# Kernel optimization log

Measured on AMD Instinct MI355X. Metric: run time of the kernel, lower is better.

## Reference

```python
import jax, jax.numpy as jnp
import numpy as np

N = 10000   # nodes
E = 160000  # edges (avg degree 16)
IN = 512
HID = 512
OUT = 512


def setup_inputs() -> dict:
    key = jax.random.key(0)
    ks = jax.random.split(key, 8)
    x = jax.random.normal(ks[0], (N, IN), dtype=jnp.float32)
    edge_index = jax.random.randint(ks[1], (2, E), 0, N, dtype=jnp.int64)
    def w(k, fi, fo):
        return jax.random.normal(k, (fi, fo), dtype=jnp.float32) * (1.0 / np.sqrt(fi)).astype(np.float32)
    return {
        "x": x,
        "edge_index": edge_index,
        "W1": w(ks[2], IN, HID), "b1": jnp.zeros((HID,), jnp.float32),
        "W2": w(ks[3], HID, HID), "b2": jnp.zeros((HID,), jnp.float32),
        "W3": w(ks[4], HID, OUT), "b3": jnp.zeros((OUT,), jnp.float32),
    }


def _gcn_norm(edge_index, n):
    # add self loops, then symmetric normalization D^{-1/2} (A+I) D^{-1/2}
    loops = jnp.arange(n, dtype=edge_index.dtype)
    row = jnp.concatenate([edge_index[0], loops])  # source
    col = jnp.concatenate([edge_index[1], loops])  # target (aggregation dim)
    deg = jax.ops.segment_sum(jnp.ones_like(col, jnp.float32), col, num_segments=n)
    dis = jnp.where(deg > 0, jax.lax.rsqrt(jnp.maximum(deg, 1.0)), 0.0)
    norm = dis[row] * dis[col]  # [E+N]
    return row, col, norm


def _gcn_layer(x, row, col, norm, W, b, n):
    h = x @ W                                    # [N, d_out] dense GEMM
    msg = h[row] * norm[:, None]                 # gather + scale, [E+N, d_out]
    out = jax.ops.segment_sum(msg, col, num_segments=n)  # scatter-add
    return out + b


def reference(x, edge_index, W1, b1, W2, b2, W3, b3):
    n = x.shape[0]
    row, col, norm = _gcn_norm(edge_index, n)
    h = _gcn_layer(x, row, col, norm, W1, b1, n)
    h = jax.nn.relu(h)  # dropout is identity in eval mode
    h = _gcn_layer(h, row, col, norm, W2, b2, n)
    h = jax.nn.relu(h)
    h = _gcn_layer(h, row, col, norm, W3, b3, n)
    return h
```

## Files before the change

kernel.cpp:

```cpp
#include <hip/hip_runtime.h>

typedef __attribute__((ext_vector_type(8))) short bf16x8;
typedef __attribute__((ext_vector_type(4))) float f32x4;

#define N_NODES 10000
#define N_EDGES 160000
#define FDIM    512
#define ELL     64
#define BM 64
#define BN 128
#define BK 64
#define TM 157
#define NGEMM (TM * 4)
#define NSCAT 625
#define NTRAN 768

__device__ __forceinline__ float bf2f(unsigned int u) {
    union { unsigned int i; float f; } v; v.i = u << 16; return v.f;
}
__device__ __forceinline__ float bfs2f(short s) {
    return bf2f((unsigned int)(unsigned short)s);
}
__device__ __forceinline__ unsigned short f2bf(float f) {
    union { float f; unsigned int u; } v; v.f = f;
    unsigned int u = v.u;
    unsigned int r = u + 0x7fffu + ((u >> 16) & 1u);
    return (unsigned short)(r >> 16);
}
__device__ __forceinline__ void gload_lds16(const void* g, void* l) {
    __builtin_amdgcn_global_load_lds(
        (const __attribute__((address_space(1))) unsigned int*)g,
        (__attribute__((address_space(3))) unsigned int*)l, 16, 0, 0);
}
__device__ __forceinline__ int wave_is_f32(const unsigned int* w) {
    unsigned int v = w[(size_t)(threadIdx.x & 63) * 1000];
    unsigned int ex = (v >> 7) & 0xFFu;
    unsigned long long inb = __ballot(ex >= 100u && ex <= 140u);
    return (__popcll(inb) >= 48) ? 0 : 1;
}

__global__ __launch_bounds__(256) void prep_v6(
        const void* __restrict__ x, const void* __restrict__ ei,
        const void* __restrict__ W1, const void* __restrict__ W2,
        const void* __restrict__ W3, unsigned short* __restrict__ Wt,
        int* __restrict__ cnt, int* __restrict__ flags) {
    int b = blockIdx.x;
    if (b < NTRAN) {
        __shared__ unsigned short tile[32][33];
        int z = b >> 8, t = b & 255;
        const void* W = (z == 0) ? W1 : (z == 1) ? W2 : W3;
        unsigned short* out = Wt + (size_t)z * FDIM * FDIM;
        int ff32 = wave_is_f32((const unsigned int*)W);
        int tx = threadIdx.x & 31, ty = threadIdx.x >> 5;
        int xcol = (t & 15) * 32 + tx;
        int y0 = (t >> 4) * 32 + ty;
        #pragma unroll
        for (int j = 0; j < 32; j += 8) {
            int idx = (y0 + j) * FDIM + xcol;
            unsigned short v = ff32 ? f2bf(((const float*)W)[idx])
                                    : ((const unsigned short*)W)[idx];
            tile[ty + j][tx] = v;
        }
        __syncthreads();
        int x2 = (t >> 4) * 32 + tx;
        int y2 = (t & 15) * 32 + ty;
        #pragma unroll
        for (int j = 0; j < 32; j += 8)
            out[(y2 + j) * FDIM + x2] = tile[tx][ty + j];
    } else if (b < NTRAN + NSCAT) {
        const unsigned long long* e64 = (const unsigned long long*)ei;
        unsigned long long v = e64[(size_t)(threadIdx.x & 63) * 2500];
        unsigned long long big = __ballot(v > 0xFFFFFFFFull);
        int i64 = (big == 0ull);
        int e = (b - NTRAN) * 256 + threadIdx.x;
        int c = i64 ? (int)((const long long*)ei)[N_EDGES + e]
                    : ((const int*)ei)[N_EDGES + e];
        atomicAdd(&cnt[c], 1);
    } else {
        if (threadIdx.x < 64) {
            const unsigned long long* e64 = (const unsigned long long*)ei;
            unsigned long long v = e64[(size_t)threadIdx.x * 2500];
            unsigned long long big = __ballot(v > 0xFFFFFFFFull);
            const unsigned int* xw = (const unsigned int*)x;
            unsigned int w = xw[(size_t)threadIdx.x * 1000];
            unsigned int ex = (w >> 7) & 0xFFu;
            unsigned long long inb = __ballot(ex >= 100u && ex <= 140u);
            if (threadIdx.x == 0) {
                flags[0] = (big == 0ull) ? 1 : 0;
                flags[1] = (__popcll(inb) >= 48) ? 0 : 1;
            }
        }
    }
}

__global__ __launch_bounds__(256) void gemm_scat_v6(
        const void* __restrict__ Ap, const unsigned short* __restrict__ Bt,
        unsigned short* __restrict__ C, int M, int a_ext,
        const int* __restrict__ flags, const void* __restrict__ ei,
        const int* __restrict__ cnt, int* __restrict__ cursor,
        int2* __restrict__ ell, int do_scatter) {
    __shared__ unsigned short As[BM * BK];
    __shared__ unsigned short Bs[BN * BK];
    if (do_scatter && blockIdx.x >= NGEMM) {
        int e = (blockIdx.x - NGEMM) * 256 + threadIdx.x;
        if (e < N_EDGES) {
            int r, c;
            if (flags[0]) {
                r = (int)((const long long*)ei)[e];
                c = (int)((const long long*)ei)[N_EDGES + e];
            } else {
                r = ((const int*)ei)[e];
                c = ((const int*)ei)[N_EDGES + e];
            }
            int slot = atomicAdd(&cursor[c], 1);
            if (slot < ELL) {
                float nrm = rsqrtf((float)((cnt[r] + 1) * (cnt[c] + 1)));
                int2 pr; pr.x = r; pr.y = __float_as_int(nrm);
                ell[(size_t)c * ELL + slot] = pr;
            }
        }
        return;
    }
    const int K = FDIM;
    const int af32 = a_ext ? flags[1] : 0;
    const int tid = threadIdx.x;
    const int t = blockIdx.x;
    const int bm = (t % TM) * BM, bn = (t / TM) * BN;
    const int lane = tid & 63, wv = tid >> 6;
    const int wm = (wv >> 1) * 32, wn = (wv & 1) * 64;
    const int lrow = lane & 15, lk = (lane >> 4) * 8;
    const unsigned short* Abf = (const unsigned short*)Ap;
    f32x4 acc[2][4] = {};

    for (int k0 = 0; k0 < K; k0 += BK) {
        if (!af32) {
            #pragma unroll
            for (int j = 0; j < 2; ++j) {
                int r0 = wv * 16 + j * 8;
                int arow = bm + r0 + (lane >> 3);
                if (arow >= M) arow = M - 1;
                gload_lds16(Abf + (size_t)arow * K + k0 + (lane & 7) * 8,
                            &As[r0 * BK]);
            }
            #pragma unroll
            for (int j = 0; j < 4; ++j) {
                int r0 = wv * 32 + j * 8;
                gload_lds16(Bt + (size_t)(bn + r0 + (lane >> 3)) * K + k0 + (lane & 7) * 8,
                            &Bs[r0 * BK]);
            }
        } else {
            #pragma unroll
            for (int j = 0; j < 4; ++j) {
                int r0 = wv * 32 + j * 8;
                gload_lds16(Bt + (size_t)(bn + r0 + (lane >> 3)) * K + k0 + (lane & 7) * 8,
                            &Bs[r0 * BK]);
            }
            #pragma unroll
            for (int i = 0; i < 2; ++i) {
                int c = tid + i * 256;
                int row = c >> 3, seg = (c & 7) * 8;
                int grow = bm + row;
                bf16x8 va = {};
                if (grow < M) {
                    const float* Af = (const float*)Ap + (size_t)grow * K + k0 + seg;
                    f32x4 lo = *(const f32x4*)Af;
                    f32x4 hi = *(const f32x4*)(Af + 4);
                    #pragma unroll
                    for (int jj = 0; jj < 4; ++jj) {
                        va[jj]     = (short)f2bf(lo[jj]);
                        va[4 + jj] = (short)f2bf(hi[jj]);
                    }
                }
                *(bf16x8*)(&As[row * BK + seg]) = va;
            }
        }
        __syncthreads();
        #pragma unroll
        for (int half = 0; half < 2; ++half) {
            bf16x8 af[2], bfr[4];
            #pragma unroll
            for (int f = 0; f < 2; ++f)
                af[f] = *(const bf16x8*)(&As[(wm + f * 16 + lrow) * BK + half * 32 + lk]);
            #pragma unroll
            for (int f = 0; f < 4; ++f)
                bfr[f] = *(const bf16x8*)(&Bs[(wn + f * 16 + lrow) * BK + half * 32 + lk]);
            #pragma unroll
            for (int fm = 0; fm < 2; ++fm)
                #pragma unroll
                for (int fn = 0; fn < 4; ++fn)
                    acc[fm][fn] = __builtin_amdgcn_mfma_f32_16x16x32_bf16(
                        af[fm], bfr[fn], acc[fm][fn], 0, 0, 0);
        }
        __syncthreads();
    }

    int crow = (lane >> 4) * 4;
    int ccol = lane & 15;
    #pragma unroll
    for (int fm = 0; fm < 2; ++fm) {
        #pragma unroll
        for (int fn = 0; fn < 4; ++fn) {
            #pragma unroll
            for (int r = 0; r < 4; ++r) {
                int row = bm + wm + fm * 16 + crow + r;
                if (row < M)
                    C[(size_t)row * FDIM + bn + wn + fn * 16 + ccol] =
                        f2bf(acc[fm][fn][r]);
            }
        }
    }
}

__global__ __launch_bounds__(256) void agg_v6(
        const unsigned short* __restrict__ g, const void* __restrict__ bias,
        const int* __restrict__ cnt, const int2* __restrict__ ell,
        void* __restrict__ out, int relu, int out_ext,
        const int* __restrict__ flags) {
    int wv = threadIdx.x >> 6, lane = threadIdx.x & 63;
    int i = blockIdx.x * 2 + (wv >> 1);
    int f = (wv & 1) * 256 + lane * 4;
    float a0 = 0.f, a1 = 0.f, a2 = 0.f, a3 = 0.f;
    int ci = cnt[i];
    int rows = (ci > ELL) ? ELL : ci;
    const int2* ep = ell + (size_t)i * ELL;
    int j = 0;
    for (; j + 4 <= rows; j += 4) {
        int2 p0 = ep[j], p1 = ep[j + 1], p2 = ep[j + 2], p3 = ep[j + 3];
        uint2 v0 = *(const uint2*)(g + (size_t)p0.x * FDIM + f);
        uint2 v1 = *(const uint2*)(g + (size_t)p1.x * FDIM + f);
        uint2 v2 = *(const uint2*)(g + (size_t)p2.x * FDIM + f);
        uint2 v3 = *(const uint2*)(g + (size_t)p3.x * FDIM + f);
        float w0 = __int_as_float(p0.y), w1 = __int_as_float(p1.y);
        float w2 = __int_as_float(p2.y), w3 = __int_as_float(p3.y);
        a0 += w0 * bf2f(v0.x & 0xffffu); a1 += w0 * bf2f(v0.x >> 16);
        a2 += w0 * bf2f(v0.y & 0xffffu); a3 += w0 * bf2f(v0.y >> 16);
        a0 += w1 * bf2f(v1.x & 0xffffu); a1 += w1 * bf2f(v1.x >> 16);
        a2 += w1 * bf2f(v1.y & 0xffffu); a3 += w1 * bf2f(v1.y >> 16);
        a0 += w2 * bf2f(v2.x & 0xffffu); a1 += w2 * bf2f(v2.x >> 16);
        a2 += w2 * bf2f(v2.y & 0xffffu); a3 += w2 * bf2f(v2.y >> 16);
        a0 += w3 * bf2f(v3.x & 0xffffu); a1 += w3 * bf2f(v3.x >> 16);
        a2 += w3 * bf2f(v3.y & 0xffffu); a3 += w3 * bf2f(v3.y >> 16);
    }
    for (; j < rows; ++j) {
        int2 pp = ep[j];
        float w = __int_as_float(pp.y);
        uint2 v = *(const uint2*)(g + (size_t)pp.x * FDIM + f);
        a0 += w * bf2f(v.x & 0xffffu); a1 += w * bf2f(v.x >> 16);
        a2 += w * bf2f(v.y & 0xffffu); a3 += w * bf2f(v.y >> 16);
    }
    float wself = 1.0f / (float)(ci + 1);
    uint2 vs = *(const uint2*)(g + (size_t)i * FDIM + f);
    a0 += wself * bf2f(vs.x & 0xffffu); a1 += wself * bf2f(vs.x >> 16);
    a2 += wself * bf2f(vs.y & 0xffffu); a3 += wself * bf2f(vs.y >> 16);
    int ff32 = flags[1];
    if (ff32) {
        f32x4 bb = *(const f32x4*)((const float*)bias + f);
        a0 += bb[0]; a1 += bb[1]; a2 += bb[2]; a3 += bb[3];
    } else {
        uint2 bb = *(const uint2*)((const unsigned short*)bias + f);
        a0 += bf2f(bb.x & 0xffffu); a1 += bf2f(bb.x >> 16);
        a2 += bf2f(bb.y & 0xffffu); a3 += bf2f(bb.y >> 16);
    }
    if (relu) {
        a0 = fmaxf(a0, 0.f); a1 = fmaxf(a1, 0.f);
        a2 = fmaxf(a2, 0.f); a3 = fmaxf(a3, 0.f);
    }
    if (out_ext && ff32) {
        f32x4 o = {a0, a1, a2, a3};
        *(f32x4*)((float*)out + (size_t)i * FDIM + f) = o;
    } else {
        uint2 o;
        o.x = (unsigned int)f2bf(a0) | ((unsigned int)f2bf(a1) << 16);
        o.y = (unsigned int)f2bf(a2) | ((unsigned int)f2bf(a3) << 16);
        *(uint2*)((unsigned short*)out + (size_t)i * FDIM + f) = o;
    }
}

extern "C" void kernel_launch(void* const* d_in, const int* in_sizes, int n_in,
                              void* d_out, int out_size, void* d_ws, size_t ws_size,
                              hipStream_t stream) {
    (void)in_sizes; (void)n_in; (void)out_size; (void)ws_size;
    const void* x  = d_in[0];
    const void* ei = d_in[1];
    const void* W1 = d_in[2];
    const void* b1 = d_in[3];
    const void* W2 = d_in[4];
    const void* b2 = d_in[5];
    const void* W3 = d_in[6];
    const void* b3 = d_in[7];

    char* p = (char*)d_ws;
    auto alloc = [&](size_t bytes) -> void* {
        void* r = (void*)p;
        p += (bytes + 255) & ~(size_t)255;
        return r;
    };
    int*  flags   = (int*) alloc(16);
    int*  cntcur  = (int*) alloc((size_t)2 * N_NODES * 4);
    int2* ell     = (int2*)alloc((size_t)N_NODES * ELL * 8);
    unsigned short* Wt = (unsigned short*)alloc((size_t)3 * FDIM * FDIM * 2);
    unsigned short* g  = (unsigned short*)alloc((size_t)N_NODES * FDIM * 2);
    int* cnt    = cntcur;
    int* cursor = cntcur + N_NODES;
    unsigned short* Wt1 = Wt;
    unsigned short* Wt2 = Wt + (size_t)FDIM * FDIM;
    unsigned short* Wt3 = Wt + (size_t)2 * FDIM * FDIM;
    unsigned short* h   = (unsigned short*)d_out;

    hipMemsetAsync(cntcur, 0, (size_t)2 * N_NODES * 4, stream);
    prep_v6<<<NTRAN + NSCAT + 1, 256, 0, stream>>>(x, ei, W1, W2, W3, Wt, cnt, flags);

    gemm_scat_v6<<<NGEMM + NSCAT, 256, 0, stream>>>(x, Wt1, g, N_NODES, 1, flags,
                                                    ei, cnt, cursor, ell, 1);
    agg_v6<<<N_NODES / 2, 256, 0, stream>>>(g, b1, cnt, ell, h, 1, 0, flags);
    gemm_scat_v6<<<NGEMM, 256, 0, stream>>>(h, Wt2, g, N_NODES, 0, flags,
                                            ei, cnt, cursor, ell, 0);
    agg_v6<<<N_NODES / 2, 256, 0, stream>>>(g, b2, cnt, ell, h, 1, 0, flags);
    gemm_scat_v6<<<NGEMM, 256, 0, stream>>>(h, Wt3, g, N_NODES, 0, flags,
                                            ei, cnt, cursor, ell, 0);
    agg_v6<<<N_NODES / 2, 256, 0, stream>>>(g, b3, cnt, ell, d_out, 0, 1, flags);
}
```

Before: 226.4 us.

## Fuse aggregation with next-layer GEMM, drop count pass, swizzle LDS

Aggregation for layers 1 and 2 now runs in the same kernel as the following GEMM. Each block aggregates 48 rows into LDS and multiplies them by the full weight matrix, so the intermediate activations are never written to and reread from global memory. The separate degree-count pass and memset are gone: the scatter counts with a single atomic cursor, and edge weights are computed on the fly from counts using shuffles, which also halves the ELL storage. The GEMM's LDS layout gets an XOR swizzle to avoid bank conflicts. In exchange, the fused kernel launches only 209 blocks with a large LDS footprint, and it reloads B tiles for every block.

```diff
diff --git a/kernel.cpp b/kernel.cpp
--- a/kernel.cpp
+++ b/kernel.cpp
@@ -14,6 +14,10 @@
 #define NGEMM (TM * 4)
 #define NSCAT 625
 #define NTRAN 768
+#define NZERO 40
+#define FBM 48
+#define FNB 209
+#define APAD 520
 
 __device__ __forceinline__ float bf2f(unsigned int u) {
     union { unsigned int i; float f; } v; v.i = u << 16; return v.f;
@@ -39,53 +43,46 @@
     return (__popcll(inb) >= 48) ? 0 : 1;
 }
 
-__global__ __launch_bounds__(256) void prep_v6(
+__global__ __launch_bounds__(256) void prep_v8(
         const void* __restrict__ x, const void* __restrict__ ei,
         const void* __restrict__ W1, const void* __restrict__ W2,
         const void* __restrict__ W3, unsigned short* __restrict__ Wt,
         int* __restrict__ cnt, int* __restrict__ flags) {
-    int b = blockIdx.x;
+    int b = blockIdx.x, tid = threadIdx.x;
     if (b < NTRAN) {
         __shared__ unsigned short tile[32][33];
         int z = b >> 8, t = b & 255;
         const void* W = (z == 0) ? W1 : (z == 1) ? W2 : W3;
-        unsigned short* out = Wt + (size_t)z * FDIM * FDIM;
+        unsigned short* outp = Wt + (size_t)z * FDIM * FDIM;
         int ff32 = wave_is_f32((const unsigned int*)W);
-        int tx = threadIdx.x & 31, ty = threadIdx.x >> 5;
+        int tx = tid & 31, ty = tid >> 5;
         int xcol = (t & 15) * 32 + tx;
         int y0 = (t >> 4) * 32 + ty;
         #pragma unroll
         for (int j = 0; j < 32; j += 8) {
             int idx = (y0 + j) * FDIM + xcol;
-            unsigned short v = ff32 ? f2bf(((const float*)W)[idx])
+            tile[ty + j][tx] = ff32 ? f2bf(((const float*)W)[idx])
                                     : ((const unsigned short*)W)[idx];
-            tile[ty + j][tx] = v;
         }
         __syncthreads();
         int x2 = (t >> 4) * 32 + tx;
         int y2 = (t & 15) * 32 + ty;
         #pragma unroll
         for (int j = 0; j < 32; j += 8)
-            out[(y2 + j) * FDIM + x2] = tile[tx][ty + j];
-    } else if (b < NTRAN + NSCAT) {
-        const unsigned long long* e64 = (const unsigned long long*)ei;
-        unsigned long long v = e64[(size_t)(threadIdx.x & 63) * 2500];
-        unsigned long long big = __ballot(v > 0xFFFFFFFFull);
-        int i64 = (big == 0ull);
-        int e = (b - NTRAN) * 256 + threadIdx.x;
-        int c = i64 ? (int)((const long long*)ei)[N_EDGES + e]
-                    : ((const int*)ei)[N_EDGES + e];
-        atomicAdd(&cnt[c], 1);
+            outp[(y2 + j) * FDIM + x2] = tile[tx][ty + j];
+    } else if (b < NTRAN + NZERO) {
+        int i = (b - NTRAN) * 256 + tid;
+        if (i < N_NODES) cnt[i] = 0;
     } else {
-        if (threadIdx.x < 64) {
+        if (tid < 64) {
             const unsigned long long* e64 = (const unsigned long long*)ei;
-            unsigned long long v = e64[(size_t)threadIdx.x * 2500];
+            unsigned long long v = e64[(size_t)tid * 2500];
             unsigned long long big = __ballot(v > 0xFFFFFFFFull);
             const unsigned int* xw = (const unsigned int*)x;
-            unsigned int w = xw[(size_t)threadIdx.x * 1000];
+            unsigned int w = xw[(size_t)tid * 1000];
             unsigned int ex = (w >> 7) & 0xFFu;
             unsigned long long inb = __ballot(ex >= 100u && ex <= 140u);
-            if (threadIdx.x == 0) {
+            if (tid == 0) {
                 flags[0] = (big == 0ull) ? 1 : 0;
                 flags[1] = (__popcll(inb) >= 48) ? 0 : 1;
             }
@@ -93,15 +90,14 @@
     }
 }
 
-__global__ __launch_bounds__(256) void gemm_scat_v6(
+__global__ __launch_bounds__(256) void gemm_scat_v8(
         const void* __restrict__ Ap, const unsigned short* __restrict__ Bt,
-        unsigned short* __restrict__ C, int M, int a_ext,
-        const int* __restrict__ flags, const void* __restrict__ ei,
-        const int* __restrict__ cnt, int* __restrict__ cursor,
-        int2* __restrict__ ell, int do_scatter) {
+        unsigned short* __restrict__ C, const int* __restrict__ flags,
+        const void* __restrict__ ei, int* __restrict__ cnt,
+        int* __restrict__ ell) {
     __shared__ unsigned short As[BM * BK];
     __shared__ unsigned short Bs[BN * BK];
-    if (do_scatter && blockIdx.x >= NGEMM) {
+    if (blockIdx.x >= NGEMM) {
         int e = (blockIdx.x - NGEMM) * 256 + threadIdx.x;
         if (e < N_EDGES) {
             int r, c;
@@ -112,23 +108,21 @@
                 r = ((const int*)ei)[e];
                 c = ((const int*)ei)[N_EDGES + e];
             }
-            int slot = atomicAdd(&cursor[c], 1);
-            if (slot < ELL) {
-                float nrm = rsqrtf((float)((cnt[r] + 1) * (cnt[c] + 1)));
-                int2 pr; pr.x = r; pr.y = __float_as_int(nrm);
-                ell[(size_t)c * ELL + slot] = pr;
-            }
+            int slot = atomicAdd(&cnt[c], 1);
+            if (slot < ELL) ell[(size_t)c * ELL + slot] = r;
         }
         return;
     }
     const int K = FDIM;
-    const int af32 = a_ext ? flags[1] : 0;
+    const int af32 = flags[1];
     const int tid = threadIdx.x;
     const int t = blockIdx.x;
     const int bm = (t % TM) * BM, bn = (t / TM) * BN;
     const int lane = tid & 63, wv = tid >> 6;
     const int wm = (wv >> 1) * 32, wn = (wv & 1) * 64;
-    const int lrow = lane & 15, lk = (lane >> 4) * 8;
+    const int lrow = lane & 15;
+    const int tsl = lane >> 4;
+    const int ksw = (lane & 7) ^ ((lane >> 3) & 7);
     const unsigned short* Abf = (const unsigned short*)Ap;
     f32x4 acc[2][4] = {};
 
@@ -138,31 +132,30 @@
             for (int j = 0; j < 2; ++j) {
                 int r0 = wv * 16 + j * 8;
                 int arow = bm + r0 + (lane >> 3);
-                if (arow >= M) arow = M - 1;
-                gload_lds16(Abf + (size_t)arow * K + k0 + (lane & 7) * 8,
-                            &As[r0 * BK]);
+                if (arow >= N_NODES) arow = N_NODES - 1;
+                gload_lds16(Abf + (size_t)arow * K + k0 + ksw * 8, &As[r0 * BK]);
             }
             #pragma unroll
             for (int j = 0; j < 4; ++j) {
                 int r0 = wv * 32 + j * 8;
-                gload_lds16(Bt + (size_t)(bn + r0 + (lane >> 3)) * K + k0 + (lane & 7) * 8,
+                gload_lds16(Bt + (size_t)(bn + r0 + (lane >> 3)) * K + k0 + ksw * 8,
                             &Bs[r0 * BK]);
             }
         } else {
             #pragma unroll
             for (int j = 0; j < 4; ++j) {
                 int r0 = wv * 32 + j * 8;
-                gload_lds16(Bt + (size_t)(bn + r0 + (lane >> 3)) * K + k0 + (lane & 7) * 8,
+                gload_lds16(Bt + (size_t)(bn + r0 + (lane >> 3)) * K + k0 + ksw * 8,
                             &Bs[r0 * BK]);
             }
             #pragma unroll
             for (int i = 0; i < 2; ++i) {
                 int c = tid + i * 256;
-                int row = c >> 3, seg = (c & 7) * 8;
+                int row = c >> 3, sl = c & 7;
                 int grow = bm + row;
                 bf16x8 va = {};
-                if (grow < M) {
-                    const float* Af = (const float*)Ap + (size_t)grow * K + k0 + seg;
+                if (grow < N_NODES) {
+                    const float* Af = (const float*)Ap + (size_t)grow * K + k0 + sl * 8;
                     f32x4 lo = *(const f32x4*)Af;
                     f32x4 hi = *(const f32x4*)(Af + 4);
                     #pragma unroll
@@ -171,19 +164,24 @@
                         va[4 + jj] = (short)f2bf(hi[jj]);
                     }
                 }
-                *(bf16x8*)(&As[row * BK + seg]) = va;
+                *(bf16x8*)(&As[row * BK + ((sl ^ (row & 7)) * 8)]) = va;
             }
         }
         __syncthreads();
         #pragma unroll
         for (int half = 0; half < 2; ++half) {
+            int ts = half * 4 + tsl;
             bf16x8 af[2], bfr[4];
             #pragma unroll
-            for (int f = 0; f < 2; ++f)
-                af[f] = *(const bf16x8*)(&As[(wm + f * 16 + lrow) * BK + half * 32 + lk]);
-            #pragma unroll
-            for (int f = 0; f < 4; ++f)
-                bfr[f] = *(const bf16x8*)(&Bs[(wn + f * 16 + lrow) * BK + half * 32 + lk]);
+            for (int f = 0; f < 2; ++f) {
+                int row = wm + f * 16 + lrow;
+                af[f] = *(const bf16x8*)(&As[row * BK + ((ts ^ (lrow & 7)) * 8)]);
+            }
+            #pragma unroll
+            for (int f = 0; f < 4; ++f) {
+                int row = wn + f * 16 + lrow;
+                bfr[f] = *(const bf16x8*)(&Bs[row * BK + ((ts ^ (lrow & 7)) * 8)]);
+            }
             #pragma unroll
             for (int fm = 0; fm < 2; ++fm)
                 #pragma unroll
@@ -197,41 +195,154 @@
     int crow = (lane >> 4) * 4;
     int ccol = lane & 15;
     #pragma unroll
-    for (int fm = 0; fm < 2; ++fm) {
-        #pragma unroll
-        for (int fn = 0; fn < 4; ++fn) {
+    for (int fm = 0; fm < 2; ++fm)
+        #pragma unroll
+        for (int fn = 0; fn < 4; ++fn)
             #pragma unroll
             for (int r = 0; r < 4; ++r) {
                 int row = bm + wm + fm * 16 + crow + r;
-                if (row < M)
+                if (row < N_NODES)
                     C[(size_t)row * FDIM + bn + wn + fn * 16 + ccol] =
                         f2bf(acc[fm][fn][r]);
             }
-        }
-    }
-}
-
-__global__ __launch_bounds__(256) void agg_v6(
+}
+
+__global__ __launch_bounds__(384) void fused_ag_v8(
+        const unsigned short* __restrict__ gin, const void* __restrict__ bias,
+        const int* __restrict__ cnt, const int* __restrict__ ell,
+        const unsigned short* __restrict__ Bt, unsigned short* __restrict__ Cout,
+        const int* __restrict__ flags) {
+    __shared__ unsigned short As[FBM * APAD];
+    __shared__ unsigned short Bs[512 * 64];
+    const int tid = threadIdx.x, lane = tid & 63, wv = tid / 64;
+    const int bm = blockIdx.x * FBM;
+    const int ff32 = flags[1];
+    const int ksw = (lane & 7) ^ ((lane >> 3) & 7);
+
+    for (int m = wv; m < 64; m += 6) {
+        int r0 = m * 8;
+        gload_lds16(Bt + (size_t)(r0 + (lane >> 3)) * FDIM + 0 + ksw * 8,
+                    &Bs[r0 * 64]);
+    }
+
+    for (int rl = wv * 8; rl < wv * 8 + 8; ++rl) {
+        int i = bm + rl;
+        float a[8] = {};
+        if (i < N_NODES) {
+            int ci = cnt[i];
+            int re = (ci > ELL) ? ELL : ci;
+            const int* ep = ell + (size_t)i * ELL;
+            int   srcl = (lane < re) ? ep[lane] : 0;
+            int   cl   = (lane < re) ? cnt[srcl] : 0;
+            float wl = rsqrtf((float)(cl + 1) * (float)(ci + 1));
+            int j = 0;
+            for (; j + 8 <= re; j += 8) {
+                int s[8]; float w[8]; bf16x8 v[8];
+                #pragma unroll
+                for (int q = 0; q < 8; ++q) {
+                    s[q] = __shfl(srcl, j + q); w[q] = __shfl(wl, j + q);
+                }
+                #pragma unroll
+                for (int q = 0; q < 8; ++q)
+                    v[q] = *(const bf16x8*)(gin + (size_t)s[q] * FDIM + lane * 8);
+                #pragma unroll
+                for (int q = 0; q < 8; ++q)
+                    #pragma unroll
+                    for (int tt = 0; tt < 8; ++tt) a[tt] += w[q] * bfs2f(v[q][tt]);
+            }
+            for (; j < re; ++j) {
+                int s = __shfl(srcl, j); float w = __shfl(wl, j);
+                bf16x8 v = *(const bf16x8*)(gin + (size_t)s * FDIM + lane * 8);
+                #pragma unroll
+                for (int tt = 0; tt < 8; ++tt) a[tt] += w * bfs2f(v[tt]);
+            }
+            float wself = 1.0f / (float)(ci + 1);
+            bf16x8 vs = *(const bf16x8*)(gin + (size_t)i * FDIM + lane * 8);
+            #pragma unroll
+            for (int tt = 0; tt < 8; ++tt) a[tt] += wself * bfs2f(vs[tt]);
+            if (ff32) {
+                const float* B = (const float*)bias + lane * 8;
+                #pragma unroll
+                for (int tt = 0; tt < 8; ++tt) a[tt] += B[tt];
+            } else {
+                bf16x8 bb = *(const bf16x8*)((const unsigned short*)bias + lane * 8);
+                #pragma unroll
+                for (int tt = 0; tt < 8; ++tt) a[tt] += bfs2f(bb[tt]);
+            }
+            #pragma unroll
+            for (int tt = 0; tt < 8; ++tt) a[tt] = fmaxf(a[tt], 0.f);
+        }
+        bf16x8 o;
+        #pragma unroll
+        for (int tt = 0; tt < 8; ++tt) o[tt] = (short)f2bf(a[tt]);
+        *(bf16x8*)(&As[rl * APAD + lane * 8]) = o;
+    }
+    __syncthreads();
+
+    const int wrow = wv % 3, wcol = wv / 3;
+    const int lrow = lane & 15, tsl = lane >> 4;
+    f32x4 acc[16] = {};
+    for (int k0 = 0; k0 < FDIM; k0 += 64) {
+        #pragma unroll
+        for (int half = 0; half < 2; ++half) {
+            bf16x8 af = *(const bf16x8*)(
+                &As[(wrow * 16 + lrow) * APAD + k0 + half * 32 + tsl * 8]);
+            int ts = half * 4 + tsl;
+            #pragma unroll
+            for (int ct = 0; ct < 16; ++ct) {
+                int n = wcol * 256 + ct * 16 + lrow;
+                bf16x8 bfr = *(const bf16x8*)(
+                    &Bs[n * 64 + ((ts ^ (lrow & 7)) * 8)]);
+                acc[ct] = __builtin_amdgcn_mfma_f32_16x16x32_bf16(
+                    af, bfr, acc[ct], 0, 0, 0);
+            }
+        }
+        __syncthreads();
+        if (k0 + 64 < FDIM) {
+            for (int m = wv; m < 64; m += 6) {
+                int r0 = m * 8;
+                gload_lds16(Bt + (size_t)(r0 + (lane >> 3)) * FDIM + (k0 + 64) + ksw * 8,
+                            &Bs[r0 * 64]);
+            }
+        }
+        __syncthreads();
+    }
+    int crow = (lane >> 4) * 4, ccol = lane & 15;
+    #pragma unroll
+    for (int ct = 0; ct < 16; ++ct)
+        #pragma unroll
+        for (int r = 0; r < 4; ++r) {
+            int grow = bm + wrow * 16 + crow + r;
+            if (grow < N_NODES)
+                Cout[(size_t)grow * FDIM + wcol * 256 + ct * 16 + ccol] =
+                    f2bf(acc[ct][r]);
+        }
+}
+
+__global__ __launch_bounds__(256) void agg3_v8(
         const unsigned short* __restrict__ g, const void* __restrict__ bias,
-        const int* __restrict__ cnt, const int2* __restrict__ ell,
-        void* __restrict__ out, int relu, int out_ext,
-        const int* __restrict__ flags) {
+        const int* __restrict__ cnt, const int* __restrict__ ell,
+        void* __restrict__ out, const int* __restrict__ flags) {
     int wv = threadIdx.x >> 6, lane = threadIdx.x & 63;
     int i = blockIdx.x * 2 + (wv >> 1);
     int f = (wv & 1) * 256 + lane * 4;
+    int ci = cnt[i];
+    int re = (ci > ELL) ? ELL : ci;
+    const int* ep = ell + (size_t)i * ELL;
+    int   srcl = (lane < re) ? ep[lane] : 0;
+    int   cl   = (lane < re) ? cnt[srcl] : 0;
+    float wl = rsqrtf((float)(cl + 1) * (float)(ci + 1));
     float a0 = 0.f, a1 = 0.f, a2 = 0.f, a3 = 0.f;
-    int ci = cnt[i];
-    int rows = (ci > ELL) ? ELL : ci;
-    const int2* ep = ell + (size_t)i * ELL;
     int j = 0;
-    for (; j + 4 <= rows; j += 4) {
-        int2 p0 = ep[j], p1 = ep[j + 1], p2 = ep[j + 2], p3 = ep[j + 3];
-        uint2 v0 = *(const uint2*)(g + (size_t)p0.x * FDIM + f);
-        uint2 v1 = *(const uint2*)(g + (size_t)p1.x * FDIM + f);
-        uint2 v2 = *(const uint2*)(g + (size_t)p2.x * FDIM + f);
-        uint2 v3 = *(const uint2*)(g + (size_t)p3.x * FDIM + f);
-        float w0 = __int_as_float(p0.y), w1 = __int_as_float(p1.y);
-        float w2 = __int_as_float(p2.y), w3 = __int_as_float(p3.y);
+    for (; j + 4 <= re; j += 4) {
+        int s0 = __shfl(srcl, j);     float w0 = __shfl(wl, j);
+        int s1 = __shfl(srcl, j + 1); float w1 = __shfl(wl, j + 1);
+        int s2 = __shfl(srcl, j + 2); float w2 = __shfl(wl, j + 2);
+        int s3 = __shfl(srcl, j + 3); float w3 = __shfl(wl, j + 3);
+        uint2 v0 = *(const uint2*)(g + (size_t)s0 * FDIM + f);
+        uint2 v1 = *(const uint2*)(g + (size_t)s1 * FDIM + f);
+        uint2 v2 = *(const uint2*)(g + (size_t)s2 * FDIM + f);
+        uint2 v3 = *(const uint2*)(g + (size_t)s3 * FDIM + f);
         a0 += w0 * bf2f(v0.x & 0xffffu); a1 += w0 * bf2f(v0.x >> 16);
         a2 += w0 * bf2f(v0.y & 0xffffu); a3 += w0 * bf2f(v0.y >> 16);
         a0 += w1 * bf2f(v1.x & 0xffffu); a1 += w1 * bf2f(v1.x >> 16);
@@ -241,10 +352,9 @@
         a0 += w3 * bf2f(v3.x & 0xffffu); a1 += w3 * bf2f(v3.x >> 16);
         a2 += w3 * bf2f(v3.y & 0xffffu); a3 += w3 * bf2f(v3.y >> 16);
     }
-    for (; j < rows; ++j) {
-        int2 pp = ep[j];
-        float w = __int_as_float(pp.y);
-        uint2 v = *(const uint2*)(g + (size_t)pp.x * FDIM + f);
+    for (; j < re; ++j) {
+        int s = __shfl(srcl, j); float w = __shfl(wl, j);
+        uint2 v = *(const uint2*)(g + (size_t)s * FDIM + f);
         a0 += w * bf2f(v.x & 0xffffu); a1 += w * bf2f(v.x >> 16);
         a2 += w * bf2f(v.y & 0xffffu); a3 += w * bf2f(v.y >> 16);
     }
@@ -256,19 +366,12 @@
     if (ff32) {
         f32x4 bb = *(const f32x4*)((const float*)bias + f);
         a0 += bb[0]; a1 += bb[1]; a2 += bb[2]; a3 += bb[3];
+        f32x4 o = {a0, a1, a2, a3};
+        *(f32x4*)((float*)out + (size_t)i * FDIM + f) = o;
     } else {
         uint2 bb = *(const uint2*)((const unsigned short*)bias + f);
         a0 += bf2f(bb.x & 0xffffu); a1 += bf2f(bb.x >> 16);
         a2 += bf2f(bb.y & 0xffffu); a3 += bf2f(bb.y >> 16);
-    }
-    if (relu) {
-        a0 = fmaxf(a0, 0.f); a1 = fmaxf(a1, 0.f);
-        a2 = fmaxf(a2, 0.f); a3 = fmaxf(a3, 0.f);
-    }
-    if (out_ext && ff32) {
-        f32x4 o = {a0, a1, a2, a3};
-        *(f32x4*)((float*)out + (size_t)i * FDIM + f) = o;
-    } else {
         uint2 o;
         o.x = (unsigned int)f2bf(a0) | ((unsigned int)f2bf(a1) << 16);
         o.y = (unsigned int)f2bf(a2) | ((unsigned int)f2bf(a3) << 16);
@@ -295,28 +398,20 @@
         p += (bytes + 255) & ~(size_t)255;
         return r;
     };
-    int*  flags   = (int*) alloc(16);
-    int*  cntcur  = (int*) alloc((size_t)2 * N_NODES * 4);
-    int2* ell     = (int2*)alloc((size_t)N_NODES * ELL * 8);
+    int*  flags = (int*) alloc(16);
+    int*  cnt   = (int*) alloc((size_t)N_NODES * 4);
+    int*  ell   = (int*) alloc((size_t)N_NODES * ELL * 4);
     unsigned short* Wt = (unsigned short*)alloc((size_t)3 * FDIM * FDIM * 2);
     unsigned short* g  = (unsigned short*)alloc((size_t)N_NODES * FDIM * 2);
-    int* cnt    = cntcur;
-    int* cursor = cntcur + N_NODES;
+
     unsigned short* Wt1 = Wt;
     unsigned short* Wt2 = Wt + (size_t)FDIM * FDIM;
     unsigned short* Wt3 = Wt + (size_t)2 * FDIM * FDIM;
     unsigned short* h   = (unsigned short*)d_out;
 
-    hipMemsetAsync(cntcur, 0, (size_t)2 * N_NODES * 4, stream);
-    prep_v6<<<NTRAN + NSCAT + 1, 256, 0, stream>>>(x, ei, W1, W2, W3, Wt, cnt, flags);
-
-    gemm_scat_v6<<<NGEMM + NSCAT, 256, 0, stream>>>(x, Wt1, g, N_NODES, 1, flags,
-                                                    ei, cnt, cursor, ell, 1);
-    agg_v6<<<N_NODES / 2, 256, 0, stream>>>(g, b1, cnt, ell, h, 1, 0, flags);
-    gemm_scat_v6<<<NGEMM, 256, 0, stream>>>(h, Wt2, g, N_NODES, 0, flags,
-                                            ei, cnt, cursor, ell, 0);
-    agg_v6<<<N_NODES / 2, 256, 0, stream>>>(g, b2, cnt, ell, h, 1, 0, flags);
-    gemm_scat_v6<<<NGEMM, 256, 0, stream>>>(h, Wt3, g, N_NODES, 0, flags,
-                                            ei, cnt, cursor, ell, 0);
-    agg_v6<<<N_NODES / 2, 256, 0, stream>>>(g, b3, cnt, ell, d_out, 0, 1, flags);
-}
+    prep_v8<<<NTRAN + NZERO + 1, 256, 0, stream>>>(x, ei, W1, W2, W3, Wt, cnt, flags);
+    gemm_scat_v8<<<NGEMM + NSCAT, 256, 0, stream>>>(x, Wt1, g, flags, ei, cnt, ell);
+    fused_ag_v8<<<FNB, 384, 0, stream>>>(g, b1, cnt, ell, Wt2, h, flags);
+    fused_ag_v8<<<FNB, 384, 0, stream>>>(h, b2, cnt, ell, Wt3, g, flags);
+    agg3_v8<<<N_NODES / 2, 256, 0, stream>>>(g, b3, cnt, ell, d_out, flags);
+}
```

Measured after the change: 228.6 us. Within noise of the previous version (+1.0%).
